# Optimization experiments

Hardware: AMD Instinct MI355X
Metric: run time of the kernel (lower is better)

Reference implementation:

```python
import jax, jax.numpy as jnp
import numpy as np

B, T, D, H = 2, 2048, 1024, 16  # batch, seq_len, d_model (d_in==d_out), num_heads
HD = D // H  # head_dim = 64


def setup_inputs() -> dict:
    key = jax.random.key(0)
    ks = jax.random.split(key, 6)
    s = 1.0 / np.sqrt(D)
    return {
        "x": jax.random.normal(ks[0], (B, T, D), dtype=jnp.float32),
        "wq": jax.random.normal(ks[1], (D, D), dtype=jnp.float32) * s,
        "wk": jax.random.normal(ks[2], (D, D), dtype=jnp.float32) * s,
        "wv": jax.random.normal(ks[3], (D, D), dtype=jnp.float32) * s,
        "wo": jax.random.normal(ks[4], (D, D), dtype=jnp.float32) * s,
        "bo": jax.random.normal(ks[5], (D,), dtype=jnp.float32) * 0.01,
    }


def reference(x, wq, wk, wv, wo, bo):
    b, t, d = x.shape
    # projections (qkv_bias=False), split heads: [b, h, t, hd]
    q = (x @ wq).reshape(b, t, H, HD).transpose(0, 2, 1, 3)
    k = (x @ wk).reshape(b, t, H, HD).transpose(0, 2, 1, 3)
    v = (x @ wv).reshape(b, t, H, HD).transpose(0, 2, 1, 3)
    # causal attention scores [b, h, t, t]
    scores = jnp.einsum("bhqd,bhkd->bhqk", q, k) / jnp.sqrt(jnp.float32(HD))
    causal = jnp.tril(jnp.ones((t, t), dtype=bool))
    scores = jnp.where(causal[None, None, :, :], scores, -jnp.inf)
    attn = jax.nn.softmax(scores, axis=-1)  # dropout p=0.0 -> identity
    ctx = jnp.einsum("bhqk,bhkd->bhqd", attn, v)  # [b, h, t, hd]
    ctx = ctx.transpose(0, 2, 1, 3).reshape(b, t, d)  # merge heads
    return ctx @ wo + bo
```

## Files before the change

kernel.cpp:

```cpp
#include <hip/hip_runtime.h>
#include <hip/hip_bf16.h>
#include <stdint.h>

#define B_  2
#define T_  2048
#define D_  1024
#define H_  16
#define HD_ 64

typedef __bf16 bf16x8 __attribute__((ext_vector_type(8)));
typedef __bf16 bf16x4 __attribute__((ext_vector_type(4)));
typedef float  f32x4  __attribute__((ext_vector_type(4)));

__device__ __forceinline__ void async_copy16(const void* g, void* l) {
  __builtin_amdgcn_global_load_lds((__attribute__((address_space(1))) void*)(g),
                                   (__attribute__((address_space(3))) void*)(l),
                                   16, 0, 0);
}

__global__ void detect_kernel(const void* __restrict__ x_raw, const void* __restrict__ bo_raw,
                              int* __restrict__ flagp, float* __restrict__ bo_f) {
  __shared__ int sh[2];
  const int tid = threadIdx.x;
  if (tid == 0) { sh[0] = 0; sh[1] = 0; }
  __syncthreads();
  const unsigned short* xw = (const unsigned short*)x_raw;
  int h = 0, z = 0;
  for (int i = tid; i < 8192; i += 256) {
    const unsigned short wv = xw[i];
    const int e = (wv >> 7) & 0xFF;
    if (e > 150) ++h;
    if (((i & 1) == 0) && (wv == 0)) ++z;
  }
  atomicAdd(&sh[0], h);
  atomicAdd(&sh[1], z);
  __syncthreads();
  const int f32 = (sh[0] > 512 || sh[1] > 1024) ? 1 : 0;
  for (int i = tid; i < 1024; i += 256)
    bo_f[i] = f32 ? ((const float*)bo_raw)[i] : (float)((const __bf16*)bo_raw)[i];
  if (tid == 0) *flagp = f32;
}

__global__ void convert_x_kernel(const void* __restrict__ x_raw, const int* __restrict__ flagp,
                                 __bf16* __restrict__ xc) {
  const int f32 = *flagp;
  const int i0 = (blockIdx.x * 256 + threadIdx.x) * 4;
  if (f32) {
    const float* xf = (const float*)x_raw;
#pragma unroll
    for (int k = 0; k < 4; ++k) xc[i0 + k] = (__bf16)xf[i0 + k];
  } else {
    *(bf16x4*)(xc + i0) = *(const bf16x4*)((const __bf16*)x_raw + i0);
  }
}

__global__ void transpose_w_kernel(const void* __restrict__ wq, const void* __restrict__ wk,
                                   const void* __restrict__ wv, const void* __restrict__ wo,
                                   const int* __restrict__ flagp,
                                   __bf16* __restrict__ wqkv_t, __bf16* __restrict__ wo_t) {
  __shared__ __bf16 tile[32][33];
  const int f32 = *flagp;
  const int z = blockIdx.z;
  const void* src = (z == 0) ? wq : (z == 1) ? wk : (z == 2) ? wv : wo;
  __bf16* dst = (z < 3) ? (wqkv_t + (size_t)z * 1024 * 1024) : wo_t;
  const int n0 = blockIdx.x * 32, k0 = blockIdx.y * 32;
  const int tx = threadIdx.x, ty = threadIdx.y;
#pragma unroll
  for (int i = 0; i < 4; ++i) {
    const size_t idx = (size_t)(k0 + ty + 8 * i) * 1024 + n0 + tx;
    tile[ty + 8 * i][tx] = f32 ? (__bf16)((const float*)src)[idx] : ((const __bf16*)src)[idx];
  }
  __syncthreads();
#pragma unroll
  for (int i = 0; i < 4; ++i)
    dst[(size_t)(n0 + ty + 8 * i) * 1024 + k0 + tx] = tile[tx][ty + 8 * i];
}

template <int MODE>
__launch_bounds__(256)
__global__ void gemm128_kernel(const __bf16* __restrict__ A, const __bf16* __restrict__ Bt, int K,
                               __bf16* __restrict__ q_b, __bf16* __restrict__ k_b,
                               __bf16* __restrict__ vt_b,
                               const float* __restrict__ bo_f, const int* __restrict__ flagp,
                               void* __restrict__ outp) {
  __shared__ __align__(16) __bf16 As[128 * 64];
  __shared__ __align__(16) __bf16 Bs[128 * 64];
  const int tid  = threadIdx.x;
  const int w    = tid >> 6, lane = tid & 63;
  const int quad = lane >> 4, lr = lane & 15;
  const int tm = blockIdx.y * 128, tn = blockIdx.x * 128;
  const int wm = (w >> 1) * 64, wn = (w & 1) * 64;
  const int lrow   = lane >> 3;
  const int gchunk = (lane & 7) ^ lrow;

  f32x4 acc[4][4] = {};

  for (int k0 = 0; k0 < K; k0 += 64) {
#pragma unroll
    for (int c = 0; c < 4; ++c) {
      const int chunk = w * 4 + c;
      const int row   = chunk * 8 + lrow;
      async_copy16(A  + (size_t)(tm + row) * K + k0 + gchunk * 8, As + chunk * 512);
      async_copy16(Bt + (size_t)(tn + row) * K + k0 + gchunk * 8, Bs + chunk * 512);
    }
    __syncthreads();
#pragma unroll
    for (int ks = 0; ks < 2; ++ks) {
      bf16x8 af[4], bfr[4];
#pragma unroll
      for (int mi = 0; mi < 4; ++mi) {
        const int row = wm + mi * 16 + lr;
        const int ch  = (ks * 4 + quad) ^ (row & 7);
        af[mi] = *(const bf16x8*)(As + row * 64 + ch * 8);
      }
#pragma unroll
      for (int ni = 0; ni < 4; ++ni) {
        const int row = wn + ni * 16 + lr;
        const int ch  = (ks * 4 + quad) ^ (row & 7);
        bfr[ni] = *(const bf16x8*)(Bs + row * 64 + ch * 8);
      }
#pragma unroll
      for (int mi = 0; mi < 4; ++mi)
#pragma unroll
        for (int ni = 0; ni < 4; ++ni)
          acc[mi][ni] = __builtin_amdgcn_mfma_f32_16x16x32_bf16(af[mi], bfr[ni], acc[mi][ni], 0, 0, 0);
    }
    __syncthreads();
  }

  if (MODE == 0) {
#pragma unroll
    for (int mi = 0; mi < 4; ++mi) {
      const int mrow0 = tm + wm + mi * 16 + quad * 4;
      const int b  = mrow0 >> 11;
      const int t0 = mrow0 & 2047;
#pragma unroll
      for (int ni = 0; ni < 4; ++ni) {
        const int ncol = tn + wn + ni * 16 + lr;
        const int mat  = ncol >> 10;
        const int nn   = ncol & 1023;
        const int h = nn >> 6, hd = nn & 63;
        if (mat == 0) {
#pragma unroll
          for (int r = 0; r < 4; ++r)
            q_b[((size_t)((b * H_ + h) * T_ + t0 + r)) * HD_ + hd] =
                (__bf16)(acc[mi][ni][r] * 0.125f);
        } else if (mat == 1) {
#pragma unroll
          for (int r = 0; r < 4; ++r)
            k_b[((size_t)((b * H_ + h) * T_ + t0 + r)) * HD_ + hd] =
                (__bf16)(acc[mi][ni][r]);
        } else {
          bf16x4 pk;
#pragma unroll
          for (int r = 0; r < 4; ++r) pk[r] = (__bf16)(acc[mi][ni][r]);
          *(bf16x4*)(vt_b + ((size_t)(b * H_ + h) * HD_ + hd) * T_ + t0) = pk;
        }
      }
    }
  } else {
    const int f32out = *flagp;
#pragma unroll
    for (int mi = 0; mi < 4; ++mi) {
      const int m0 = tm + wm + mi * 16 + quad * 4;
#pragma unroll
      for (int ni = 0; ni < 4; ++ni) {
        const int n = tn + wn + ni * 16 + lr;
        const float bias = bo_f[n];
#pragma unroll
        for (int r = 0; r < 4; ++r) {
          const float val = acc[mi][ni][r] + bias;
          if (f32out) ((float*)outp)[(size_t)(m0 + r) * D_ + n] = val;
          else        ((__bf16*)outp)[(size_t)(m0 + r) * D_ + n] = (__bf16)val;
        }
      }
    }
  }
}

__launch_bounds__(256)
__global__ void attn_kernel(const __bf16* __restrict__ q_b, const __bf16* __restrict__ k_b,
                            const __bf16* __restrict__ vt_b, __bf16* __restrict__ ctx) {
  __shared__ __align__(16) __bf16 sK[64 * 64];
  __shared__ __align__(16) __bf16 sV[64 * 64];
  __shared__ __align__(16) __bf16 sP[4][2][16][72];
  const int tid  = threadIdx.x;
  const int w    = tid >> 6, lane = tid & 63;
  const int quad = lane >> 4, lr = lane & 15;
  const int bh = blockIdx.y;
  const int bx = blockIdx.x;
  const __bf16* qh = q_b  + (size_t)bh * T_ * HD_;
  const __bf16* kh = k_b  + (size_t)bh * T_ * HD_;
  const __bf16* vh = vt_b + (size_t)bh * HD_ * T_;
  const int b = bh >> 4, h = bh & 15;

  const int r0 = tid >> 3, r1 = (tid + 256) >> 3;
  const int g0 = tid & 7;

#pragma unroll
  for (int half = 0; half < 2; ++half) {
    const int tq = half ? (31 - bx) : bx;
    const int q0 = tq * 64 + w * 16;
    const int nj = tq + 1;

    bf16x8 qf[2];
#pragma unroll
    for (int ks = 0; ks < 2; ++ks)
      qf[ks] = *(const bf16x8*)(qh + (size_t)(q0 + lr) * HD_ + ks * 32 + quad * 8);

    f32x4 o[4] = {};
    float lsum[4] = {0.f, 0.f, 0.f, 0.f};

    bf16x8 kr0 = *(const bf16x8*)(kh + (size_t)r0 * HD_ + g0 * 8);
    bf16x8 kr1 = *(const bf16x8*)(kh + (size_t)r1 * HD_ + g0 * 8);
    bf16x8 vr0 = *(const bf16x8*)(vh + (size_t)r0 * T_ + g0 * 8);
    bf16x8 vr1 = *(const bf16x8*)(vh + (size_t)r1 * T_ + g0 * 8);

    for (int j = 0; j < nj; ++j) {
      const int j0 = j * 64;
      const int pb = j & 1;
      __syncthreads();
      *(bf16x8*)(sK + r0 * 64 + (g0 ^ (r0 & 7)) * 8) = kr0;
      *(bf16x8*)(sK + r1 * 64 + (g0 ^ (r1 & 7)) * 8) = kr1;
      *(bf16x8*)(sV + r0 * 64 + (g0 ^ (r0 & 7)) * 8) = vr0;
      *(bf16x8*)(sV + r1 * 64 + (g0 ^ (r1 & 7)) * 8) = vr1;
      __syncthreads();
      if (j + 1 < nj) {
        const int jn = j0 + 64;
        kr0 = *(const bf16x8*)(kh + (size_t)(jn + r0) * HD_ + g0 * 8);
        kr1 = *(const bf16x8*)(kh + (size_t)(jn + r1) * HD_ + g0 * 8);
        vr0 = *(const bf16x8*)(vh + (size_t)r0 * T_ + jn + g0 * 8);
        vr1 = *(const bf16x8*)(vh + (size_t)r1 * T_ + jn + g0 * 8);
      }
      f32x4 s[4] = {};
#pragma unroll
      for (int ni = 0; ni < 4; ++ni) {
        const int row = ni * 16 + lr;
#pragma unroll
        for (int ks = 0; ks < 2; ++ks) {
          const int ch = (ks * 4 + quad) ^ (row & 7);
          bf16x8 kf = *(const bf16x8*)(sK + row * 64 + ch * 8);
          s[ni] = __builtin_amdgcn_mfma_f32_16x16x32_bf16(qf[ks], kf, s[ni], 0, 0, 0);
        }
      }
      if (j0 + 63 > q0) {
#pragma unroll
        for (int ni = 0; ni < 4; ++ni) {
          const int col = j0 + ni * 16 + lr;
#pragma unroll
          for (int r = 0; r < 4; ++r) {
            const int row = q0 + quad * 4 + r;
            if (col > row) s[ni][r] = -3.0e38f;
          }
        }
      }
#pragma unroll
      for (int ni = 0; ni < 4; ++ni)
#pragma unroll
        for (int r = 0; r < 4; ++r)
          s[ni][r] = __expf(s[ni][r]);
#pragma unroll
      for (int r = 0; r < 4; ++r)
        lsum[r] += (s[0][r] + s[1][r]) + (s[2][r] + s[3][r]);
#pragma unroll
      for (int ni = 0; ni < 4; ++ni)
#pragma unroll
        for (int r = 0; r < 4; ++r)
          sP[w][pb][quad * 4 + r][ni * 16 + lr] = (__bf16)s[ni][r];
      asm volatile("s_waitcnt lgkmcnt(0)" ::: "memory");
      bf16x8 pf[2];
#pragma unroll
      for (int ks = 0; ks < 2; ++ks)
        pf[ks] = *(const bf16x8*)(&sP[w][pb][lr][ks * 32 + quad * 8]);
#pragma unroll
      for (int ni = 0; ni < 4; ++ni) {
        const int row = ni * 16 + lr;
#pragma unroll
        for (int ks = 0; ks < 2; ++ks) {
          const int ch = (ks * 4 + quad) ^ (row & 7);
          bf16x8 vf = *(const bf16x8*)(sV + row * 64 + ch * 8);
          o[ni] = __builtin_amdgcn_mfma_f32_16x16x32_bf16(pf[ks], vf, o[ni], 0, 0, 0);
        }
      }
    }
#pragma unroll
    for (int off = 1; off <= 8; off <<= 1)
#pragma unroll
      for (int r = 0; r < 4; ++r)
        lsum[r] += __shfl_xor(lsum[r], off, 16);
#pragma unroll
    for (int r = 0; r < 4; ++r) {
      const float inv = 1.0f / lsum[r];
      const int t = q0 + quad * 4 + r;
#pragma unroll
      for (int ni = 0; ni < 4; ++ni)
        ctx[((size_t)(b * T_ + t)) * D_ + h * HD_ + ni * 16 + lr] =
            (__bf16)(o[ni][r] * inv);
    }
  }
}

extern "C" void kernel_launch(void* const* d_in, const int* in_sizes, int n_in,
                              void* d_out, int out_size, void* d_ws, size_t ws_size,
                              hipStream_t stream) {
  (void)in_sizes; (void)n_in; (void)out_size; (void)ws_size;
  const void* x  = d_in[0];
  const void* wq = d_in[1];
  const void* wk = d_in[2];
  const void* wv = d_in[3];
  const void* wo = d_in[4];
  const void* bo = d_in[5];

  char* ws = (char*)d_ws;
  __bf16* ctx    = (__bf16*)(ws + 0);
  __bf16* wqkv_t = (__bf16*)(ws + 0);
  __bf16* wo_t   = (__bf16*)(ws + 8388608);
  __bf16* q_b    = (__bf16*)(ws + 10485760);
  __bf16* k_b    = (__bf16*)(ws + 18874368);
  __bf16* vt_b   = (__bf16*)(ws + 27262976);
  __bf16* xc     = (__bf16*)(ws + 35651584);
  float*  bo_f   = (float*) (ws + 44040192);
  int*    flagp  = (int*)   (ws + 44044288);

  detect_kernel<<<1, 256, 0, stream>>>(x, bo, flagp, bo_f);
  convert_x_kernel<<<4096, 256, 0, stream>>>(x, flagp, xc);
  transpose_w_kernel<<<dim3(32, 32, 4), dim3(32, 8, 1), 0, stream>>>(wq, wk, wv, wo, flagp, wqkv_t, wo_t);
  gemm128_kernel<0><<<dim3(24, 32), 256, 0, stream>>>(xc, wqkv_t, 1024, q_b, k_b, vt_b, nullptr, flagp, nullptr);
  attn_kernel<<<dim3(16, 32), 256, 0, stream>>>(q_b, k_b, vt_b, ctx);
  gemm128_kernel<1><<<dim3(8, 32), 256, 0, stream>>>(ctx, wo_t, 1024, nullptr, nullptr, nullptr, bo_f, flagp, d_out);
}
```

Before: 205.9 us.

## Read K/V fragments directly from global memory and remap attention block order

Drops the shared-memory staging of K and V tiles, along with its two block barriers per iteration and the register prefetch. Each wave now loads its MFMA K and V fragments straight from global memory and relies on L1/L2 caching, since all four waves read the same tile. The grid is flattened to 1D and remapped so consecutive blocks cover different heads, which is meant to spread heads across XCDs and L2 slices. The cost is four times more global/L1 load traffic per tile and global latency exposed directly ahead of each MFMA, with no software prefetch.

```diff
diff --git a/kernel.cpp b/kernel.cpp
--- a/kernel.cpp
+++ b/kernel.cpp
@@ -181,22 +181,18 @@
 __launch_bounds__(256)
 __global__ void attn_kernel(const __bf16* __restrict__ q_b, const __bf16* __restrict__ k_b,
                             const __bf16* __restrict__ vt_b, __bf16* __restrict__ ctx) {
-  __shared__ __align__(16) __bf16 sK[64 * 64];
-  __shared__ __align__(16) __bf16 sV[64 * 64];
   __shared__ __align__(16) __bf16 sP[4][2][16][72];
   const int tid  = threadIdx.x;
   const int w    = tid >> 6, lane = tid & 63;
   const int quad = lane >> 4, lr = lane & 15;
-  const int bh = blockIdx.y;
-  const int bx = blockIdx.x;
+  const int id = blockIdx.x;
+  const int bh = (id & 7) * 4 + ((id >> 3) & 3);
+  const int bx = id >> 5;
   const __bf16* qh = q_b  + (size_t)bh * T_ * HD_;
   const __bf16* kh = k_b  + (size_t)bh * T_ * HD_;
   const __bf16* vh = vt_b + (size_t)bh * HD_ * T_;
   const int b = bh >> 4, h = bh & 15;
 
-  const int r0 = tid >> 3, r1 = (tid + 256) >> 3;
-  const int g0 = tid & 7;
-
 #pragma unroll
   for (int half = 0; half < 2; ++half) {
     const int tq = half ? (31 - bx) : bx;
@@ -211,35 +207,15 @@
     f32x4 o[4] = {};
     float lsum[4] = {0.f, 0.f, 0.f, 0.f};
 
-    bf16x8 kr0 = *(const bf16x8*)(kh + (size_t)r0 * HD_ + g0 * 8);
-    bf16x8 kr1 = *(const bf16x8*)(kh + (size_t)r1 * HD_ + g0 * 8);
-    bf16x8 vr0 = *(const bf16x8*)(vh + (size_t)r0 * T_ + g0 * 8);
-    bf16x8 vr1 = *(const bf16x8*)(vh + (size_t)r1 * T_ + g0 * 8);
-
     for (int j = 0; j < nj; ++j) {
       const int j0 = j * 64;
       const int pb = j & 1;
-      __syncthreads();
-      *(bf16x8*)(sK + r0 * 64 + (g0 ^ (r0 & 7)) * 8) = kr0;
-      *(bf16x8*)(sK + r1 * 64 + (g0 ^ (r1 & 7)) * 8) = kr1;
-      *(bf16x8*)(sV + r0 * 64 + (g0 ^ (r0 & 7)) * 8) = vr0;
-      *(bf16x8*)(sV + r1 * 64 + (g0 ^ (r1 & 7)) * 8) = vr1;
-      __syncthreads();
-      if (j + 1 < nj) {
-        const int jn = j0 + 64;
-        kr0 = *(const bf16x8*)(kh + (size_t)(jn + r0) * HD_ + g0 * 8);
-        kr1 = *(const bf16x8*)(kh + (size_t)(jn + r1) * HD_ + g0 * 8);
-        vr0 = *(const bf16x8*)(vh + (size_t)r0 * T_ + jn + g0 * 8);
-        vr1 = *(const bf16x8*)(vh + (size_t)r1 * T_ + jn + g0 * 8);
-      }
       f32x4 s[4] = {};
 #pragma unroll
       for (int ni = 0; ni < 4; ++ni) {
-        const int row = ni * 16 + lr;
 #pragma unroll
         for (int ks = 0; ks < 2; ++ks) {
-          const int ch = (ks * 4 + quad) ^ (row & 7);
-          bf16x8 kf = *(const bf16x8*)(sK + row * 64 + ch * 8);
+          bf16x8 kf = *(const bf16x8*)(kh + (size_t)(j0 + ni * 16 + lr) * HD_ + ks * 32 + quad * 8);
           s[ni] = __builtin_amdgcn_mfma_f32_16x16x32_bf16(qf[ks], kf, s[ni], 0, 0, 0);
         }
       }
@@ -274,11 +250,9 @@
         pf[ks] = *(const bf16x8*)(&sP[w][pb][lr][ks * 32 + quad * 8]);
 #pragma unroll
       for (int ni = 0; ni < 4; ++ni) {
-        const int row = ni * 16 + lr;
 #pragma unroll
         for (int ks = 0; ks < 2; ++ks) {
-          const int ch = (ks * 4 + quad) ^ (row & 7);
-          bf16x8 vf = *(const bf16x8*)(sV + row * 64 + ch * 8);
+          bf16x8 vf = *(const bf16x8*)(vh + (size_t)(ni * 16 + lr) * T_ + j0 + ks * 32 + quad * 8);
           o[ni] = __builtin_amdgcn_mfma_f32_16x16x32_bf16(pf[ks], vf, o[ni], 0, 0, 0);
         }
       }
@@ -326,6 +300,6 @@
   convert_x_kernel<<<4096, 256, 0, stream>>>(x, flagp, xc);
   transpose_w_kernel<<<dim3(32, 32, 4), dim3(32, 8, 1), 0, stream>>>(wq, wk, wv, wo, flagp, wqkv_t, wo_t);
   gemm128_kernel<0><<<dim3(24, 32), 256, 0, stream>>>(xc, wqkv_t, 1024, q_b, k_b, vt_b, nullptr, flagp, nullptr);
-  attn_kernel<<<dim3(16, 32), 256, 0, stream>>>(q_b, k_b, vt_b, ctx);
+  attn_kernel<<<512, 256, 0, stream>>>(q_b, k_b, vt_b, ctx);
   gemm128_kernel<1><<<dim3(8, 32), 256, 0, stream>>>(ctx, wo_t, 1024, nullptr, nullptr, nullptr, bo_f, flagp, d_out);
 }
```

New measurement: 279.4 us. +35.7%, slower.

## Restructure causal attention into 2-wave blocks with per-block single query tile

Applied to the files above, without the earlier changes.

The attention kernel now runs 128-thread blocks of two waves, each wave owning 32 query rows (two 16-row MFMA tiles) so every K/V fragment read from LDS feeds two MFMAs. Each block handles one 64-row query tile instead of pairing a tile with its mirror, and the grid becomes 1024 blocks. A remapped block index spreads heads and balances causal tile lengths across the launch order. This aims to raise occupancy and LDS reuse, at the cost of more registers per wave, more blocks each reloading K/V, and per-block causal work that is no longer balanced within a block.

```diff
diff --git a/kernel.cpp b/kernel.cpp
--- a/kernel.cpp
+++ b/kernel.cpp
@@ -178,126 +178,151 @@
   }
 }
 
-__launch_bounds__(256)
+__launch_bounds__(128)
 __global__ void attn_kernel(const __bf16* __restrict__ q_b, const __bf16* __restrict__ k_b,
                             const __bf16* __restrict__ vt_b, __bf16* __restrict__ ctx) {
   __shared__ __align__(16) __bf16 sK[64 * 64];
   __shared__ __align__(16) __bf16 sV[64 * 64];
-  __shared__ __align__(16) __bf16 sP[4][2][16][72];
+  __shared__ __align__(16) __bf16 sP[2][2][2][16][72];
   const int tid  = threadIdx.x;
   const int w    = tid >> 6, lane = tid & 63;
   const int quad = lane >> 4, lr = lane & 15;
-  const int bh = blockIdx.y;
-  const int bx = blockIdx.x;
+  const int id  = blockIdx.x;
+  const int bh  = (id & 7) * 4 + ((id >> 3) & 3);
+  const int raw = id >> 5;
+  const int g   = raw & 7, sidx = raw >> 3;
+  const int tq  = (sidx == 0) ? g : (sidx == 1) ? (31 - g) : (sidx == 2) ? (g + 8) : (23 - g);
   const __bf16* qh = q_b  + (size_t)bh * T_ * HD_;
   const __bf16* kh = k_b  + (size_t)bh * T_ * HD_;
   const __bf16* vh = vt_b + (size_t)bh * HD_ * T_;
   const int b = bh >> 4, h = bh & 15;
 
-  const int r0 = tid >> 3, r1 = (tid + 256) >> 3;
-  const int g0 = tid & 7;
-
-#pragma unroll
-  for (int half = 0; half < 2; ++half) {
-    const int tq = half ? (31 - bx) : bx;
-    const int q0 = tq * 64 + w * 16;
-    const int nj = tq + 1;
-
-    bf16x8 qf[2];
+  const int q0 = tq * 64 + w * 32;
+  const int nj = tq + 1;
+
+  bf16x8 qf[2][2];
+#pragma unroll
+  for (int mi = 0; mi < 2; ++mi)
 #pragma unroll
     for (int ks = 0; ks < 2; ++ks)
-      qf[ks] = *(const bf16x8*)(qh + (size_t)(q0 + lr) * HD_ + ks * 32 + quad * 8);
-
-    f32x4 o[4] = {};
-    float lsum[4] = {0.f, 0.f, 0.f, 0.f};
-
-    bf16x8 kr0 = *(const bf16x8*)(kh + (size_t)r0 * HD_ + g0 * 8);
-    bf16x8 kr1 = *(const bf16x8*)(kh + (size_t)r1 * HD_ + g0 * 8);
-    bf16x8 vr0 = *(const bf16x8*)(vh + (size_t)r0 * T_ + g0 * 8);
-    bf16x8 vr1 = *(const bf16x8*)(vh + (size_t)r1 * T_ + g0 * 8);
-
-    for (int j = 0; j < nj; ++j) {
-      const int j0 = j * 64;
-      const int pb = j & 1;
-      __syncthreads();
-      *(bf16x8*)(sK + r0 * 64 + (g0 ^ (r0 & 7)) * 8) = kr0;
-      *(bf16x8*)(sK + r1 * 64 + (g0 ^ (r1 & 7)) * 8) = kr1;
-      *(bf16x8*)(sV + r0 * 64 + (g0 ^ (r0 & 7)) * 8) = vr0;
-      *(bf16x8*)(sV + r1 * 64 + (g0 ^ (r1 & 7)) * 8) = vr1;
-      __syncthreads();
-      if (j + 1 < nj) {
-        const int jn = j0 + 64;
-        kr0 = *(const bf16x8*)(kh + (size_t)(jn + r0) * HD_ + g0 * 8);
-        kr1 = *(const bf16x8*)(kh + (size_t)(jn + r1) * HD_ + g0 * 8);
-        vr0 = *(const bf16x8*)(vh + (size_t)r0 * T_ + jn + g0 * 8);
-        vr1 = *(const bf16x8*)(vh + (size_t)r1 * T_ + jn + g0 * 8);
-      }
-      f32x4 s[4] = {};
-#pragma unroll
-      for (int ni = 0; ni < 4; ++ni) {
-        const int row = ni * 16 + lr;
-#pragma unroll
-        for (int ks = 0; ks < 2; ++ks) {
-          const int ch = (ks * 4 + quad) ^ (row & 7);
-          bf16x8 kf = *(const bf16x8*)(sK + row * 64 + ch * 8);
-          s[ni] = __builtin_amdgcn_mfma_f32_16x16x32_bf16(qf[ks], kf, s[ni], 0, 0, 0);
-        }
-      }
-      if (j0 + 63 > q0) {
+      qf[mi][ks] = *(const bf16x8*)(qh + (size_t)(q0 + mi * 16 + lr) * HD_ + ks * 32 + quad * 8);
+
+  f32x4 o[2][4] = {};
+  float lsum[2][4] = {};
+
+  bf16x8 kr[4], vr[4];
+#pragma unroll
+  for (int i = 0; i < 4; ++i) {
+    const int cid = i * 128 + tid;
+    const int row = cid >> 3, gg = cid & 7;
+    kr[i] = *(const bf16x8*)(kh + (size_t)row * HD_ + gg * 8);
+    vr[i] = *(const bf16x8*)(vh + (size_t)row * T_ + gg * 8);
+  }
+
+  for (int j = 0; j < nj; ++j) {
+    const int j0 = j * 64;
+    const int pb = j & 1;
+    __syncthreads();
+#pragma unroll
+    for (int i = 0; i < 4; ++i) {
+      const int cid = i * 128 + tid;
+      const int row = cid >> 3, gg = cid & 7;
+      *(bf16x8*)(sK + row * 64 + (gg ^ (row & 7)) * 8) = kr[i];
+      *(bf16x8*)(sV + row * 64 + (gg ^ (row & 7)) * 8) = vr[i];
+    }
+    __syncthreads();
+    if (j + 1 < nj) {
+      const int jn = j0 + 64;
+#pragma unroll
+      for (int i = 0; i < 4; ++i) {
+        const int cid = i * 128 + tid;
+        const int row = cid >> 3, gg = cid & 7;
+        kr[i] = *(const bf16x8*)(kh + (size_t)(jn + row) * HD_ + gg * 8);
+        vr[i] = *(const bf16x8*)(vh + (size_t)row * T_ + jn + gg * 8);
+      }
+    }
+    f32x4 s[2][4] = {};
+#pragma unroll
+    for (int ni = 0; ni < 4; ++ni) {
+      const int row = ni * 16 + lr;
+#pragma unroll
+      for (int ks = 0; ks < 2; ++ks) {
+        const int ch = (ks * 4 + quad) ^ (row & 7);
+        bf16x8 kf = *(const bf16x8*)(sK + row * 64 + ch * 8);
+#pragma unroll
+        for (int mi = 0; mi < 2; ++mi)
+          s[mi][ni] = __builtin_amdgcn_mfma_f32_16x16x32_bf16(qf[mi][ks], kf, s[mi][ni], 0, 0, 0);
+      }
+    }
+    if (j0 + 63 > q0) {
+#pragma unroll
+      for (int mi = 0; mi < 2; ++mi)
 #pragma unroll
         for (int ni = 0; ni < 4; ++ni) {
           const int col = j0 + ni * 16 + lr;
 #pragma unroll
           for (int r = 0; r < 4; ++r) {
-            const int row = q0 + quad * 4 + r;
-            if (col > row) s[ni][r] = -3.0e38f;
+            const int row = q0 + mi * 16 + quad * 4 + r;
+            if (col > row) s[mi][ni][r] = -3.0e38f;
           }
         }
-      }
+    }
+#pragma unroll
+    for (int mi = 0; mi < 2; ++mi) {
 #pragma unroll
       for (int ni = 0; ni < 4; ++ni)
 #pragma unroll
         for (int r = 0; r < 4; ++r)
-          s[ni][r] = __expf(s[ni][r]);
+          s[mi][ni][r] = __expf(s[mi][ni][r]);
 #pragma unroll
       for (int r = 0; r < 4; ++r)
-        lsum[r] += (s[0][r] + s[1][r]) + (s[2][r] + s[3][r]);
+        lsum[mi][r] += (s[mi][0][r] + s[mi][1][r]) + (s[mi][2][r] + s[mi][3][r]);
+    }
+#pragma unroll
+    for (int mi = 0; mi < 2; ++mi)
 #pragma unroll
       for (int ni = 0; ni < 4; ++ni)
 #pragma unroll
         for (int r = 0; r < 4; ++r)
-          sP[w][pb][quad * 4 + r][ni * 16 + lr] = (__bf16)s[ni][r];
-      asm volatile("s_waitcnt lgkmcnt(0)" ::: "memory");
-      bf16x8 pf[2];
+          sP[w][pb][mi][quad * 4 + r][ni * 16 + lr] = (__bf16)s[mi][ni][r];
+    asm volatile("s_waitcnt lgkmcnt(0)" ::: "memory");
+    bf16x8 pf[2][2];
+#pragma unroll
+    for (int mi = 0; mi < 2; ++mi)
 #pragma unroll
       for (int ks = 0; ks < 2; ++ks)
-        pf[ks] = *(const bf16x8*)(&sP[w][pb][lr][ks * 32 + quad * 8]);
-#pragma unroll
-      for (int ni = 0; ni < 4; ++ni) {
-        const int row = ni * 16 + lr;
-#pragma unroll
-        for (int ks = 0; ks < 2; ++ks) {
-          const int ch = (ks * 4 + quad) ^ (row & 7);
-          bf16x8 vf = *(const bf16x8*)(sV + row * 64 + ch * 8);
-          o[ni] = __builtin_amdgcn_mfma_f32_16x16x32_bf16(pf[ks], vf, o[ni], 0, 0, 0);
-        }
-      }
-    }
-#pragma unroll
-    for (int off = 1; off <= 8; off <<= 1)
+        pf[mi][ks] = *(const bf16x8*)(&sP[w][pb][mi][lr][ks * 32 + quad * 8]);
+#pragma unroll
+    for (int ni = 0; ni < 4; ++ni) {
+      const int row = ni * 16 + lr;
+#pragma unroll
+      for (int ks = 0; ks < 2; ++ks) {
+        const int ch = (ks * 4 + quad) ^ (row & 7);
+        bf16x8 vf = *(const bf16x8*)(sV + row * 64 + ch * 8);
+#pragma unroll
+        for (int mi = 0; mi < 2; ++mi)
+          o[mi][ni] = __builtin_amdgcn_mfma_f32_16x16x32_bf16(pf[mi][ks], vf, o[mi][ni], 0, 0, 0);
+      }
+    }
+  }
+#pragma unroll
+  for (int off = 1; off <= 8; off <<= 1)
+#pragma unroll
+    for (int mi = 0; mi < 2; ++mi)
 #pragma unroll
       for (int r = 0; r < 4; ++r)
-        lsum[r] += __shfl_xor(lsum[r], off, 16);
+        lsum[mi][r] += __shfl_xor(lsum[mi][r], off, 16);
+#pragma unroll
+  for (int mi = 0; mi < 2; ++mi)
 #pragma unroll
     for (int r = 0; r < 4; ++r) {
-      const float inv = 1.0f / lsum[r];
-      const int t = q0 + quad * 4 + r;
+      const float inv = 1.0f / lsum[mi][r];
+      const int t = q0 + mi * 16 + quad * 4 + r;
 #pragma unroll
       for (int ni = 0; ni < 4; ++ni)
         ctx[((size_t)(b * T_ + t)) * D_ + h * HD_ + ni * 16 + lr] =
-            (__bf16)(o[ni][r] * inv);
-    }
-  }
+            (__bf16)(o[mi][ni][r] * inv);
+    }
 }
 
 extern "C" void kernel_launch(void* const* d_in, const int* in_sizes, int n_in,
@@ -326,6 +351,6 @@
   convert_x_kernel<<<4096, 256, 0, stream>>>(x, flagp, xc);
   transpose_w_kernel<<<dim3(32, 32, 4), dim3(32, 8, 1), 0, stream>>>(wq, wk, wv, wo, flagp, wqkv_t, wo_t);
   gemm128_kernel<0><<<dim3(24, 32), 256, 0, stream>>>(xc, wqkv_t, 1024, q_b, k_b, vt_b, nullptr, flagp, nullptr);
-  attn_kernel<<<dim3(16, 32), 256, 0, stream>>>(q_b, k_b, vt_b, ctx);
+  attn_kernel<<<1024, 128, 0, stream>>>(q_b, k_b, vt_b, ctx);
   gemm128_kernel<1><<<dim3(8, 32), 256, 0, stream>>>(ctx, wo_t, 1024, nullptr, nullptr, nullptr, bo_f, flagp, d_out);
 }
```

After: 205.8 us. About the same (-0.0%).
